# Kernel optimization log

Hardware: AMD Instinct MI355X
Metric: run time of the kernel (lower is better)

## Reference

```python
import jax, jax.numpy as jnp
import numpy as np

LUT_DIM = 33
CTX_DIM = 128


def _identity_lut(dim):
    coords = jnp.linspace(0.0, 1.0, dim)
    r, g, b = jnp.meshgrid(coords, coords, coords, indexing='ij')
    return jnp.stack([r, g, b], axis=-1)  # [dim, dim, dim, 3], axes (r,g,b)


def setup_inputs() -> dict:
    key = jax.random.key(0)
    ks = jax.random.split(key, 8)
    B, H, W = 4, 512, 512
    image = jax.random.normal(ks[0], (B, 3, H, W), dtype=jnp.float32)
    spatial_context = jax.random.normal(ks[1], (B, CTX_DIM, H, W), dtype=jnp.float32)
    s = 0.05
    params = {
        'base_lut': _identity_lut(LUT_DIM),
        'W1': jax.random.normal(ks[2], (128, CTX_DIM), dtype=jnp.float32) * s,
        'b1': jnp.zeros((128,), dtype=jnp.float32),
        'W2': jax.random.normal(ks[3], (64, 128), dtype=jnp.float32) * s,
        'b2': jnp.zeros((64,), dtype=jnp.float32),
        'W3': jax.random.normal(ks[4], (3, 64), dtype=jnp.float32) * s,
        'b3': jnp.zeros((3,), dtype=jnp.float32),
        'offset_scale': jnp.float32(0.1),
    }
    return {'image': image, 'spatial_context': spatial_context, **params}


def _conv1x1(x, W, b):
    # x: [B,Cin,H,W], W: [Cout,Cin]
    return jnp.einsum('bchw,oc->bohw', x, W) + b[None, :, None, None]


def _trilinear_lut(lut_flat, gx, gy, gz, dim):
    # lut_flat: [3, dim^3] (flattened over z,y,x = r,g,b axes)
    # gx,gy,gz: [B,H,W] float coords in [0, dim-1]; border padding via clamp
    fmax = jnp.float32(dim - 1)
    gx = jnp.clip(gx, 0.0, fmax)
    gy = jnp.clip(gy, 0.0, fmax)
    gz = jnp.clip(gz, 0.0, fmax)
    x0 = jnp.floor(gx).astype(jnp.int32)
    y0 = jnp.floor(gy).astype(jnp.int32)
    z0 = jnp.floor(gz).astype(jnp.int32)
    x1 = jnp.minimum(x0 + 1, dim - 1)
    y1 = jnp.minimum(y0 + 1, dim - 1)
    z1 = jnp.minimum(z0 + 1, dim - 1)
    fx = gx - x0.astype(gx.dtype)
    fy = gy - y0.astype(gy.dtype)
    fz = gz - z0.astype(gz.dtype)

    def gather(zi, yi, xi):
        idx = (zi * dim + yi) * dim + xi  # [B,H,W]
        return lut_flat[:, idx]  # [3,B,H,W]

    c000 = gather(z0, y0, x0); c001 = gather(z0, y0, x1)
    c010 = gather(z0, y1, x0); c011 = gather(z0, y1, x1)
    c100 = gather(z1, y0, x0); c101 = gather(z1, y0, x1)
    c110 = gather(z1, y1, x0); c111 = gather(z1, y1, x1)

    fx = fx[None]; fy = fy[None]; fz = fz[None]
    c00 = c000 * (1 - fx) + c001 * fx
    c01 = c010 * (1 - fx) + c011 * fx
    c10 = c100 * (1 - fx) + c101 * fx
    c11 = c110 * (1 - fx) + c111 * fx
    c0 = c00 * (1 - fy) + c01 * fy
    c1 = c10 * (1 - fy) + c11 * fy
    out = c0 * (1 - fz) + c1 * fz  # [3,B,H,W]
    return jnp.transpose(out, (1, 0, 2, 3))  # [B,3,H,W]


def reference(image, spatial_context, base_lut, W1, b1, W2, b2, W3, b3, offset_scale):
    dim = base_lut.shape[0]
    gelu = lambda v: jax.nn.gelu(v, approximate=False)
    h = gelu(_conv1x1(spatial_context, W1, b1))
    h = gelu(_conv1x1(h, W2, b2))
    offset = jnp.tanh(_conv1x1(h, W3, b3)) * offset_scale  # [B,3,H,W]

    img01 = jnp.clip((image + 1.0) * 0.5, 0.0, 1.0)
    # grid_sample convention: grid channel0 (R)->x->last LUT axis (b),
    # channel1 (G)->y->g axis, channel2 (B)->z->r axis; align_corners=True.
    scale = jnp.float32(dim - 1)
    gx = img01[:, 0] * scale  # R -> b axis
    gy = img01[:, 1] * scale  # G -> g axis
    gz = img01[:, 2] * scale  # B -> r axis
    # base_lut [r,g,b,3] -> channels-first [3, r(=z), g(=y), b(=x)] -> flatten
    lut_flat = jnp.transpose(base_lut, (3, 0, 1, 2)).reshape(3, dim * dim * dim)
    sampled = _trilinear_lut(lut_flat, gx, gy, gz, dim)  # [B,3,H,W]
    return sampled * 2.0 - 1.0 + offset
```

## Files before the change

### kernel.cpp

```cpp
#include <hip/hip_runtime.h>
#include <stdint.h>

#define HW 262144
#define LDIM 33

typedef __bf16 bf16x8 __attribute__((ext_vector_type(8)));
typedef __bf16 bf16x2 __attribute__((ext_vector_type(2)));
typedef float  f32x4  __attribute__((ext_vector_type(4)));

union BF8 { bf16x8 v; unsigned u[4]; };

__device__ __forceinline__ unsigned pk2(float a, float b) {
  bf16x2 p; p[0] = (__bf16)a; p[1] = (__bf16)b;
  return __builtin_bit_cast(unsigned, p);
}
__device__ __forceinline__ float tanh_fast(float x) {
  return 1.0f - 2.0f / (__expf(2.0f * x) + 1.0f);
}
__device__ __forceinline__ float gelu_t(float x) {
  float t = tanh_fast(0.7978845608028654f * (x + 0.044715f * x * x * x));
  return 0.5f * x * (1.0f + t);
}

struct F3 { float x, y, z; };
__device__ __forceinline__ F3 lerp3(F3 a, F3 b, float f) {
  F3 r; r.x = a.x + f * (b.x - a.x); r.y = a.y + f * (b.y - a.y);
  r.z = a.z + f * (b.z - a.z); return r;
}

__global__ __launch_bounds__(512, 4) void local3dlut_kernel(
    const float* __restrict__ img,  const float* __restrict__ ctx,
    const float* __restrict__ lut,  const float* __restrict__ W1,
    const float* __restrict__ b1,   const float* __restrict__ W2,
    const float* __restrict__ b2,   const float* __restrict__ W3,
    const float* __restrict__ b3,   const float* __restrict__ oscp,
    float* __restrict__ out)
{
  __shared__ uint4 smem4[5120];
  char* sm = (char*)smem4;
  const int t    = threadIdx.x;
  const int lane = t & 63;
  const int wv   = t >> 6;
  const int n    = lane & 15;
  const int q    = lane >> 4;

  #pragma unroll
  for (int rep = 0; rep < 8; ++rep) {
    int f4 = t + 512 * rep;
    float4 v = ((const float4*)W1)[f4];
    int fi = f4 << 2;
    int o = fi >> 7, k = fi & 127;
    char* dst = sm + o * 256 + (((k >> 3) ^ (o & 15)) << 4) + ((k & 7) << 1);
    *(uint2*)dst = make_uint2(pk2(v.x, v.y), pk2(v.z, v.w));
  }
  #pragma unroll
  for (int rep = 0; rep < 4; ++rep) {
    int f4 = t + 512 * rep;
    float4 v = ((const float4*)W2)[f4];
    int fi = f4 << 2;
    int o = fi >> 7, k = fi & 127;
    char* dst = sm + 32768 + o * 256 + (((k >> 3) ^ (o & 15)) << 4) + ((k & 7) << 1);
    *(uint2*)dst = make_uint2(pk2(v.x, v.y), pk2(v.z, v.w));
  }
  __syncthreads();

  float b1r[8], b2r[4], w3r[3][4];
  #pragma unroll
  for (int i = 0; i < 8; ++i) b1r[i] = b1[i * 16 + n];
  #pragma unroll
  for (int i = 0; i < 4; ++i) b2r[i] = b2[i * 16 + n];
  #pragma unroll
  for (int j = 0; j < 3; ++j)
    #pragma unroll
    for (int i = 0; i < 4; ++i) w3r[j][i] = W3[j * 64 + i * 16 + n];
  const float b3r0 = b3[0], b3r1 = b3[1], b3r2 = b3[2];
  const float osc  = oscp[0];

  const int p0   = blockIdx.x * 1024;
  const int bi   = p0 >> 18;
  const int sblk = p0 & (HW - 1);
  const float* ctxB = ctx + (size_t)bi * ((size_t)128 * HW);
  const float* imgB = img + (size_t)bi * ((size_t)3 * HW);
  float*       outB = out + (size_t)bi * ((size_t)3 * HW);
  char* hb = sm + 49152 + wv * 4096;

  #pragma unroll 1
  for (int it = 0; it < 4; ++it) {
    const int sw = sblk + it * 256 + wv * 32;

    const int spf = sw + (lane & 31);
    const float rr = imgB[spf];
    const float gg = imgB[HW + spf];
    const float bb = imgB[2 * HW + spf];

    BF8 a1[2][4];
    #pragma unroll
    for (int mt = 0; mt < 2; ++mt) {
      const int sA = sw + mt * 16 + n;
      #pragma unroll
      for (int ks = 0; ks < 4; ++ks) {
        const float* cb = ctxB + (size_t)(ks * 32 + q * 8) * HW + sA;
        float v0 = cb[0];
        float v1 = cb[(size_t)1 * HW];
        float v2 = cb[(size_t)2 * HW];
        float v3 = cb[(size_t)3 * HW];
        float v4 = cb[(size_t)4 * HW];
        float v5 = cb[(size_t)5 * HW];
        float v6 = cb[(size_t)6 * HW];
        float v7 = cb[(size_t)7 * HW];
        a1[mt][ks].u[0] = pk2(v0, v1);
        a1[mt][ks].u[1] = pk2(v2, v3);
        a1[mt][ks].u[2] = pk2(v4, v5);
        a1[mt][ks].u[3] = pk2(v6, v7);
      }
    }

    f32x4 acc2[2][4];
    #pragma unroll
    for (int mt = 0; mt < 2; ++mt)
      #pragma unroll
      for (int j = 0; j < 4; ++j) { f32x4 z = {0.f,0.f,0.f,0.f}; acc2[mt][j] = z; }

    #pragma unroll
    for (int half = 0; half < 2; ++half) {
      f32x4 acc1[2][4];
      #pragma unroll
      for (int mt = 0; mt < 2; ++mt)
        #pragma unroll
        for (int j = 0; j < 4; ++j) { f32x4 z = {0.f,0.f,0.f,0.f}; acc1[mt][j] = z; }

      #pragma unroll
      for (int ks = 0; ks < 4; ++ks) {
        #pragma unroll
        for (int nt4 = 0; nt4 < 4; ++nt4) {
          int row = (half * 4 + nt4) * 16 + n;
          bf16x8 bw = *(const bf16x8*)(sm + row * 256 + ((((ks << 2) + q) ^ n) << 4));
          acc1[0][nt4] = __builtin_amdgcn_mfma_f32_16x16x32_bf16(a1[0][ks].v, bw, acc1[0][nt4], 0, 0, 0);
          acc1[1][nt4] = __builtin_amdgcn_mfma_f32_16x16x32_bf16(a1[1][ks].v, bw, acc1[1][nt4], 0, 0, 0);
        }
      }
      #pragma unroll
      for (int mt = 0; mt < 2; ++mt)
        #pragma unroll
        for (int nt4 = 0; nt4 < 4; ++nt4) {
          int fl = nt4 * 16 + n;
          int kgf = fl >> 3;
          #pragma unroll
          for (int r = 0; r < 4; ++r) {
            int px = mt * 16 + (q << 2) + r;
            float hv = gelu_t(acc1[mt][nt4][r] + b1r[half * 4 + nt4]);
            *(__bf16*)(hb + px * 128 + ((kgf ^ (px & 7)) << 4) + ((fl & 7) << 1)) = (__bf16)hv;
          }
        }
      #pragma unroll
      for (int ks2 = 0; ks2 < 2; ++ks2) {
        bf16x8 a2[2];
        #pragma unroll
        for (int mt = 0; mt < 2; ++mt) {
          int px = mt * 16 + n;
          a2[mt] = *(const bf16x8*)(hb + px * 128 + ((((ks2 << 2) + q) ^ (px & 7)) << 4));
        }
        #pragma unroll
        for (int nt2 = 0; nt2 < 4; ++nt2) {
          int row = nt2 * 16 + n;
          int kg2 = half * 8 + (ks2 << 2) + q;
          bf16x8 bw = *(const bf16x8*)(sm + 32768 + row * 256 + ((kg2 ^ n) << 4));
          acc2[0][nt2] = __builtin_amdgcn_mfma_f32_16x16x32_bf16(a2[0], bw, acc2[0][nt2], 0, 0, 0);
          acc2[1][nt2] = __builtin_amdgcn_mfma_f32_16x16x32_bf16(a2[1], bw, acc2[1][nt2], 0, 0, 0);
        }
      }
    }

    #pragma unroll
    for (int mt = 0; mt < 2; ++mt)
      #pragma unroll
      for (int nt2 = 0; nt2 < 4; ++nt2)
        #pragma unroll
        for (int r = 0; r < 4; ++r)
          acc2[mt][nt2][r] = gelu_t(acc2[mt][nt2][r] + b2r[nt2]);

    #pragma unroll
    for (int mt = 0; mt < 2; ++mt)
      #pragma unroll
      for (int r = 0; r < 4; ++r) {
        float h0 = acc2[mt][0][r], h1v = acc2[mt][1][r], h2v = acc2[mt][2][r], h3v = acc2[mt][3][r];
        float pa = w3r[0][0]*h0 + w3r[0][1]*h1v + w3r[0][2]*h2v + w3r[0][3]*h3v;
        float pb = w3r[1][0]*h0 + w3r[1][1]*h1v + w3r[1][2]*h2v + w3r[1][3]*h3v;
        float pc = w3r[2][0]*h0 + w3r[2][1]*h1v + w3r[2][2]*h2v + w3r[2][3]*h3v;
        pa += __shfl_xor(pa, 1, 16); pa += __shfl_xor(pa, 2, 16);
        pa += __shfl_xor(pa, 4, 16); pa += __shfl_xor(pa, 8, 16);
        pb += __shfl_xor(pb, 1, 16); pb += __shfl_xor(pb, 2, 16);
        pb += __shfl_xor(pb, 4, 16); pb += __shfl_xor(pb, 8, 16);
        pc += __shfl_xor(pc, 1, 16); pc += __shfl_xor(pc, 2, 16);
        pc += __shfl_xor(pc, 4, 16); pc += __shfl_xor(pc, 8, 16);
        int px = mt * 16 + (q << 2) + r;
        float sel  = (n == 0) ? pa   : ((n == 1) ? pb   : pc);
        float bsel = (n == 0) ? b3r0 : ((n == 1) ? b3r1 : b3r2);
        float ov = tanh_fast(sel + bsel) * osc;
        if (n < 3) *(float*)(hb + px * 12 + (n << 2)) = ov;
      }

    if (lane < 32) {
      const int sp = sw + lane;
      float o0 = *(const float*)(hb + lane * 12 + 0);
      float o1 = *(const float*)(hb + lane * 12 + 4);
      float o2 = *(const float*)(hb + lane * 12 + 8);

      float gx = fminf(fmaxf((rr + 1.f) * 0.5f, 0.f), 1.f) * 32.f;
      float gy = fminf(fmaxf((gg + 1.f) * 0.5f, 0.f), 1.f) * 32.f;
      float gz = fminf(fmaxf((bb + 1.f) * 0.5f, 0.f), 1.f) * 32.f;
      int x0 = (int)gx, y0 = (int)gy, z0 = (int)gz;
      float fx = gx - (float)x0, fy = gy - (float)y0, fz = gz - (float)z0;
      int x1 = min(x0 + 1, 32), y1 = min(y0 + 1, 32), z1 = min(z0 + 1, 32);
      int zy00 = (z0 * LDIM + y0) * LDIM, zy01 = (z0 * LDIM + y1) * LDIM;
      int zy10 = (z1 * LDIM + y0) * LDIM, zy11 = (z1 * LDIM + y1) * LDIM;
      const F3* L3 = (const F3*)lut;
      F3 c000 = L3[zy00 + x0], c001 = L3[zy00 + x1];
      F3 c010 = L3[zy01 + x0], c011 = L3[zy01 + x1];
      F3 c100 = L3[zy10 + x0], c101 = L3[zy10 + x1];
      F3 c110 = L3[zy11 + x0], c111 = L3[zy11 + x1];
      F3 c00 = lerp3(c000, c001, fx), c01 = lerp3(c010, c011, fx);
      F3 c10 = lerp3(c100, c101, fx), c11 = lerp3(c110, c111, fx);
      F3 ca  = lerp3(c00, c01, fy),   cb2 = lerp3(c10, c11, fy);
      F3 so  = lerp3(ca, cb2, fz);
      outB[sp]          = so.x * 2.f - 1.f + o0;
      outB[HW + sp]     = so.y * 2.f - 1.f + o1;
      outB[2 * HW + sp] = so.z * 2.f - 1.f + o2;
    }
  }
}

extern "C" void kernel_launch(void* const* d_in, const int* in_sizes, int n_in,
                              void* d_out, int out_size, void* d_ws, size_t ws_size,
                              hipStream_t stream) {
  const float* img = (const float*)d_in[0];
  const float* ctx = (const float*)d_in[1];
  const float* lut = (const float*)d_in[2];
  const float* W1  = (const float*)d_in[3];
  const float* b1  = (const float*)d_in[4];
  const float* W2  = (const float*)d_in[5];
  const float* b2  = (const float*)d_in[6];
  const float* W3  = (const float*)d_in[7];
  const float* b3  = (const float*)d_in[8];
  const float* osc = (const float*)d_in[9];
  float* out = (float*)d_out;
  local3dlut_kernel<<<dim3(1024), dim3(512), 0, stream>>>(
      img, ctx, lut, W1, b1, W2, b2, W3, b3, osc, out);
}
```

Before: 923.2 us.

## Halve per-wave pixel tile to 16 to cut registers and LDS

Each wave now handles 16 pixels per iteration instead of 32, with twice as many iterations. The M-tile dimension of the MFMA pipeline is dropped, so the A-fragments, accumulators and per-wave LDS staging buffer are all halved, and total shared memory shrinks. The aim is lower register and LDS pressure so more waves can be resident. In exchange, each weight fragment read from LDS feeds only one MFMA instead of two, which doubles LDS weight traffic per pixel, and the LUT stage uses only 16 of 64 lanes.

```diff
diff --git a/kernel.cpp b/kernel.cpp
--- a/kernel.cpp
+++ b/kernel.cpp
@@ -36,7 +36,7 @@
     const float* __restrict__ b3,   const float* __restrict__ oscp,
     float* __restrict__ out)
 {
-  __shared__ uint4 smem4[5120];
+  __shared__ uint4 smem4[4096];
   char* sm = (char*)smem4;
   const int t    = threadIdx.x;
   const int lane = t & 63;
@@ -82,21 +82,20 @@
   const float* ctxB = ctx + (size_t)bi * ((size_t)128 * HW);
   const float* imgB = img + (size_t)bi * ((size_t)3 * HW);
   float*       outB = out + (size_t)bi * ((size_t)3 * HW);
-  char* hb = sm + 49152 + wv * 4096;
+  char* hb = sm + 49152 + wv * 2048;
 
   #pragma unroll 1
-  for (int it = 0; it < 4; ++it) {
-    const int sw = sblk + it * 256 + wv * 32;
-
-    const int spf = sw + (lane & 31);
+  for (int it = 0; it < 8; ++it) {
+    const int sw = sblk + it * 128 + wv * 16;
+
+    const int spf = sw + n;
     const float rr = imgB[spf];
     const float gg = imgB[HW + spf];
     const float bb = imgB[2 * HW + spf];
 
-    BF8 a1[2][4];
-    #pragma unroll
-    for (int mt = 0; mt < 2; ++mt) {
-      const int sA = sw + mt * 16 + n;
+    BF8 a1[4];
+    {
+      const int sA = sw + n;
       #pragma unroll
       for (int ks = 0; ks < 4; ++ks) {
         const float* cb = ctxB + (size_t)(ks * 32 + q * 8) * HW + sA;
@@ -108,26 +107,22 @@
         float v5 = cb[(size_t)5 * HW];
         float v6 = cb[(size_t)6 * HW];
         float v7 = cb[(size_t)7 * HW];
-        a1[mt][ks].u[0] = pk2(v0, v1);
-        a1[mt][ks].u[1] = pk2(v2, v3);
-        a1[mt][ks].u[2] = pk2(v4, v5);
-        a1[mt][ks].u[3] = pk2(v6, v7);
-      }
-    }
-
-    f32x4 acc2[2][4];
-    #pragma unroll
-    for (int mt = 0; mt < 2; ++mt)
-      #pragma unroll
-      for (int j = 0; j < 4; ++j) { f32x4 z = {0.f,0.f,0.f,0.f}; acc2[mt][j] = z; }
+        a1[ks].u[0] = pk2(v0, v1);
+        a1[ks].u[1] = pk2(v2, v3);
+        a1[ks].u[2] = pk2(v4, v5);
+        a1[ks].u[3] = pk2(v6, v7);
+      }
+    }
+
+    f32x4 acc2[4];
+    #pragma unroll
+    for (int j = 0; j < 4; ++j) { f32x4 z = {0.f,0.f,0.f,0.f}; acc2[j] = z; }
 
     #pragma unroll
     for (int half = 0; half < 2; ++half) {
-      f32x4 acc1[2][4];
-      #pragma unroll
-      for (int mt = 0; mt < 2; ++mt)
-        #pragma unroll
-        for (int j = 0; j < 4; ++j) { f32x4 z = {0.f,0.f,0.f,0.f}; acc1[mt][j] = z; }
+      f32x4 acc1[4];
+      #pragma unroll
+      for (int j = 0; j < 4; ++j) { f32x4 z = {0.f,0.f,0.f,0.f}; acc1[j] = z; }
 
       #pragma unroll
       for (int ks = 0; ks < 4; ++ks) {
@@ -135,72 +130,59 @@
         for (int nt4 = 0; nt4 < 4; ++nt4) {
           int row = (half * 4 + nt4) * 16 + n;
           bf16x8 bw = *(const bf16x8*)(sm + row * 256 + ((((ks << 2) + q) ^ n) << 4));
-          acc1[0][nt4] = __builtin_amdgcn_mfma_f32_16x16x32_bf16(a1[0][ks].v, bw, acc1[0][nt4], 0, 0, 0);
-          acc1[1][nt4] = __builtin_amdgcn_mfma_f32_16x16x32_bf16(a1[1][ks].v, bw, acc1[1][nt4], 0, 0, 0);
+          acc1[nt4] = __builtin_amdgcn_mfma_f32_16x16x32_bf16(a1[ks].v, bw, acc1[nt4], 0, 0, 0);
         }
       }
       #pragma unroll
-      for (int mt = 0; mt < 2; ++mt)
+      for (int nt4 = 0; nt4 < 4; ++nt4) {
+        int fl = nt4 * 16 + n;
+        int kgf = fl >> 3;
         #pragma unroll
-        for (int nt4 = 0; nt4 < 4; ++nt4) {
-          int fl = nt4 * 16 + n;
-          int kgf = fl >> 3;
-          #pragma unroll
-          for (int r = 0; r < 4; ++r) {
-            int px = mt * 16 + (q << 2) + r;
-            float hv = gelu_t(acc1[mt][nt4][r] + b1r[half * 4 + nt4]);
-            *(__bf16*)(hb + px * 128 + ((kgf ^ (px & 7)) << 4) + ((fl & 7) << 1)) = (__bf16)hv;
-          }
+        for (int r = 0; r < 4; ++r) {
+          int px = (q << 2) + r;
+          float hv = gelu_t(acc1[nt4][r] + b1r[half * 4 + nt4]);
+          *(__bf16*)(hb + px * 128 + ((kgf ^ (px & 7)) << 4) + ((fl & 7) << 1)) = (__bf16)hv;
         }
+      }
       #pragma unroll
       for (int ks2 = 0; ks2 < 2; ++ks2) {
-        bf16x8 a2[2];
-        #pragma unroll
-        for (int mt = 0; mt < 2; ++mt) {
-          int px = mt * 16 + n;
-          a2[mt] = *(const bf16x8*)(hb + px * 128 + ((((ks2 << 2) + q) ^ (px & 7)) << 4));
-        }
+        bf16x8 a2 = *(const bf16x8*)(hb + n * 128 + ((((ks2 << 2) + q) ^ (n & 7)) << 4));
         #pragma unroll
         for (int nt2 = 0; nt2 < 4; ++nt2) {
           int row = nt2 * 16 + n;
           int kg2 = half * 8 + (ks2 << 2) + q;
           bf16x8 bw = *(const bf16x8*)(sm + 32768 + row * 256 + ((kg2 ^ n) << 4));
-          acc2[0][nt2] = __builtin_amdgcn_mfma_f32_16x16x32_bf16(a2[0], bw, acc2[0][nt2], 0, 0, 0);
-          acc2[1][nt2] = __builtin_amdgcn_mfma_f32_16x16x32_bf16(a2[1], bw, acc2[1][nt2], 0, 0, 0);
+          acc2[nt2] = __builtin_amdgcn_mfma_f32_16x16x32_bf16(a2, bw, acc2[nt2], 0, 0, 0);
         }
       }
     }
 
     #pragma unroll
-    for (int mt = 0; mt < 2; ++mt)
-      #pragma unroll
-      for (int nt2 = 0; nt2 < 4; ++nt2)
-        #pragma unroll
-        for (int r = 0; r < 4; ++r)
-          acc2[mt][nt2][r] = gelu_t(acc2[mt][nt2][r] + b2r[nt2]);
-
-    #pragma unroll
-    for (int mt = 0; mt < 2; ++mt)
-      #pragma unroll
-      for (int r = 0; r < 4; ++r) {
-        float h0 = acc2[mt][0][r], h1v = acc2[mt][1][r], h2v = acc2[mt][2][r], h3v = acc2[mt][3][r];
-        float pa = w3r[0][0]*h0 + w3r[0][1]*h1v + w3r[0][2]*h2v + w3r[0][3]*h3v;
-        float pb = w3r[1][0]*h0 + w3r[1][1]*h1v + w3r[1][2]*h2v + w3r[1][3]*h3v;
-        float pc = w3r[2][0]*h0 + w3r[2][1]*h1v + w3r[2][2]*h2v + w3r[2][3]*h3v;
-        pa += __shfl_xor(pa, 1, 16); pa += __shfl_xor(pa, 2, 16);
-        pa += __shfl_xor(pa, 4, 16); pa += __shfl_xor(pa, 8, 16);
-        pb += __shfl_xor(pb, 1, 16); pb += __shfl_xor(pb, 2, 16);
-        pb += __shfl_xor(pb, 4, 16); pb += __shfl_xor(pb, 8, 16);
-        pc += __shfl_xor(pc, 1, 16); pc += __shfl_xor(pc, 2, 16);
-        pc += __shfl_xor(pc, 4, 16); pc += __shfl_xor(pc, 8, 16);
-        int px = mt * 16 + (q << 2) + r;
-        float sel  = (n == 0) ? pa   : ((n == 1) ? pb   : pc);
-        float bsel = (n == 0) ? b3r0 : ((n == 1) ? b3r1 : b3r2);
-        float ov = tanh_fast(sel + bsel) * osc;
-        if (n < 3) *(float*)(hb + px * 12 + (n << 2)) = ov;
-      }
-
-    if (lane < 32) {
+    for (int nt2 = 0; nt2 < 4; ++nt2)
+      #pragma unroll
+      for (int r = 0; r < 4; ++r)
+        acc2[nt2][r] = gelu_t(acc2[nt2][r] + b2r[nt2]);
+
+    #pragma unroll
+    for (int r = 0; r < 4; ++r) {
+      float h0 = acc2[0][r], h1v = acc2[1][r], h2v = acc2[2][r], h3v = acc2[3][r];
+      float pa = w3r[0][0]*h0 + w3r[0][1]*h1v + w3r[0][2]*h2v + w3r[0][3]*h3v;
+      float pb = w3r[1][0]*h0 + w3r[1][1]*h1v + w3r[1][2]*h2v + w3r[1][3]*h3v;
+      float pc = w3r[2][0]*h0 + w3r[2][1]*h1v + w3r[2][2]*h2v + w3r[2][3]*h3v;
+      pa += __shfl_xor(pa, 1, 16); pa += __shfl_xor(pa, 2, 16);
+      pa += __shfl_xor(pa, 4, 16); pa += __shfl_xor(pa, 8, 16);
+      pb += __shfl_xor(pb, 1, 16); pb += __shfl_xor(pb, 2, 16);
+      pb += __shfl_xor(pb, 4, 16); pb += __shfl_xor(pb, 8, 16);
+      pc += __shfl_xor(pc, 1, 16); pc += __shfl_xor(pc, 2, 16);
+      pc += __shfl_xor(pc, 4, 16); pc += __shfl_xor(pc, 8, 16);
+      int px = (q << 2) + r;
+      float sel  = (n == 0) ? pa   : ((n == 1) ? pb   : pc);
+      float bsel = (n == 0) ? b3r0 : ((n == 1) ? b3r1 : b3r2);
+      float ov = tanh_fast(sel + bsel) * osc;
+      if (n < 3) *(float*)(hb + px * 12 + (n << 2)) = ov;
+    }
+
+    if (lane < 16) {
       const int sp = sw + lane;
       float o0 = *(const float*)(hb + lane * 12 + 0);
       float o1 = *(const float*)(hb + lane * 12 + 4);
```

Measured after the change: 1.131 ms. 1.22x slower.
